# Performance work log

Hardware: AMD Instinct MI355X
Metric: run time of the kernel (lower is better)

The kernel has to match this reference:

```python
import jax, jax.numpy as jnp
import numpy as np

N, E, F_IN, H_MID, D_OUT = 20000, 320000, 1024, 256, 128
SCALE_PARAM = 3.0
LEAKY_SLOPE = 0.01


def setup_inputs() -> dict:
    key = jax.random.key(0)
    ks = jax.random.split(key, 12)
    inv = lambda k, i, o: jax.random.normal(k, (i, o), jnp.float32) / np.sqrt(i)
    return {
        "x": jax.random.normal(ks[0], (N, F_IN), jnp.float32),
        "edge_index": jax.random.randint(ks[1], (2, E), 0, N, dtype=jnp.int64),
        "W_gcn": inv(ks[2], F_IN, H_MID),
        "b_gcn": jnp.zeros((H_MID,), jnp.float32),
        "Wq": inv(ks[3], H_MID, D_OUT), "bq": jnp.zeros((D_OUT,), jnp.float32),
        "Wk": inv(ks[4], H_MID, D_OUT), "bk": jnp.zeros((D_OUT,), jnp.float32),
        "Wv": inv(ks[5], H_MID, D_OUT), "bv": jnp.zeros((D_OUT,), jnp.float32),
        "Ws": inv(ks[6], H_MID, D_OUT), "bs": jnp.zeros((D_OUT,), jnp.float32),
    }


def reference(x, edge_index, W_gcn, b_gcn, Wq, bq, Wk, bk, Wv, bv, Ws, bs):
    n = x.shape[0]
    src, dst = edge_index[0], edge_index[1]  # message flows src(j) -> dst(i)

    # ---- GCNConv(feature_dim -> inter_dim), add_self_loops=True, sym norm ----
    loop = jnp.arange(n, dtype=src.dtype)
    row = jnp.concatenate([src, loop])
    col = jnp.concatenate([dst, loop])
    deg = jax.ops.segment_sum(jnp.ones(row.shape, x.dtype), col, num_segments=n)
    dinv = jnp.where(deg > 0, jax.lax.rsqrt(deg), 0.0)
    norm = dinv[row] * dinv[col]                      # [E+N]
    h = x @ W_gcn                                     # [N, H_MID]
    h = jax.ops.segment_sum(h[row] * norm[:, None], col, num_segments=n) + b_gcn
    h = jnp.where(h >= 0, h, LEAKY_SLOPE * h)         # LeakyReLU
    # Dropout(p) is identity at inference.

    # ---- TransformerConvReducrLayer (heads=1, no self loops, sigmoid score) ----
    d = Wq.shape[1]
    q = h @ Wq + bq
    k = h @ Wk + bk
    v = h @ Wv + bv
    alpha = jnp.sum(q[dst] * k[src], axis=-1) / jnp.sqrt(jnp.asarray(d, h.dtype))  # [E]
    alpha = alpha - alpha.mean()
    alpha = alpha / ((1.0 / SCALE_PARAM) * jnp.std(alpha, ddof=1))  # torch unbiased std
    alpha = jax.nn.sigmoid(alpha)
    msg = v[src] * alpha[:, None]                     # [E, D_OUT]
    out = jax.ops.segment_sum(msg, dst, num_segments=n)
    out = out + (h @ Ws + bs)                         # root_weight skip (PyG default)
    return out
```

## Files before the change

### kernel.cpp

```cpp
#include <hip/hip_runtime.h>
#include <hip/hip_bf16.h>

#define NNODES 20000
#define EEDGES 320000
#define FIN 1024
#define HMID 256
#define DOUT 128
#define ALPHA_BLOCKS ((NNODES + 3) / 4)

typedef __bf16 bf16x8 __attribute__((ext_vector_type(8)));
typedef __bf16 bf16x4 __attribute__((ext_vector_type(4)));
typedef __bf16 bf16x2 __attribute__((ext_vector_type(2)));
typedef float f32x4 __attribute__((ext_vector_type(4)));

typedef const __attribute__((address_space(1))) void* gas_ptr;
typedef __attribute__((address_space(3))) void* las_ptr;
__device__ __forceinline__ void async_copy16(const void* g, void* l) {
    __builtin_amdgcn_global_load_lds((gas_ptr)g, (las_ptr)l, 16, 0, 0);
}

__device__ __forceinline__ float readlane_f(float v, int lane) {
    return __uint_as_float(__builtin_amdgcn_readlane(__float_as_uint(v), lane));
}

__global__ void k_pack_w(const float* __restrict__ W, __bf16* __restrict__ Wtp) {
    int tid = blockIdx.x * 256 + threadIdx.x;
    int kk = tid >> 10;
    int rem = tid & 1023;
    int h = rem >> 9;
    int u = rem & 511;
    int kq = u >> 7, c = u & 127;
    int col = h * 128 + c;
    int k0 = kk * 32 + kq * 8;
    bf16x8 v;
#pragma unroll
    for (int j = 0; j < 8; j++)
        v[j] = (__bf16)W[(size_t)(k0 + j) * HMID + col];
    *(bf16x8*)(Wtp + (size_t)tid * 8) = v;
}

__global__ void k_prep_watt(const float* __restrict__ Wq, const float* __restrict__ Wk,
                            const float* __restrict__ Wv, const float* __restrict__ Ws,
                            const float* __restrict__ bq, const float* __restrict__ bk,
                            const float* __restrict__ bv, const float* __restrict__ bs,
                            __bf16* __restrict__ Wallt, float* __restrict__ ball) {
    int g = blockIdx.y;
    const float* W = (g == 0) ? Wq : (g == 1) ? Wk : (g == 2) ? Wv : Ws;
    int tid = blockIdx.x * 256 + threadIdx.x;
    int n = tid & 127;
    int k0u = tid >> 7;
    if (k0u < 32) {
        bf16x8 v;
#pragma unroll
        for (int j = 0; j < 8; j++)
            v[j] = (__bf16)W[(size_t)(k0u * 8 + j) * DOUT + n];
        *(bf16x8*)(Wallt + (size_t)(g * DOUT + n) * HMID + k0u * 8) = v;
    }
    if (tid < DOUT) {
        const float* b = (g == 0) ? bq : (g == 1) ? bk : (g == 2) ? bv : bs;
        ball[g * DOUT + tid] = b[tid];
    }
}

__global__ void k_init(int* __restrict__ cnt, float* __restrict__ S) {
    int i = blockIdx.x * 256 + threadIdx.x;
    if (i < NNODES) cnt[i] = 0;
    if (i < 16) S[i] = 0.0f;
}

__global__ void k_count(const int* __restrict__ dst, int* __restrict__ cnt) {
    int e = blockIdx.x * 256 + threadIdx.x;
    if (e < EEDGES) atomicAdd(&cnt[dst[e]], 1);
}

__global__ void k_dinv(const int* __restrict__ cnt, float* __restrict__ dinv,
                       int* __restrict__ cursor) {
    int i = blockIdx.x * 256 + threadIdx.x;
    if (i < NNODES) {
        dinv[i] = rsqrtf((float)cnt[i] + 1.0f);
        cursor[i] = 0;
    }
}

__global__ __launch_bounds__(1024) void k_scan(const int* __restrict__ cnt,
                                               int* __restrict__ rowptr) {
    __shared__ int sh[1024];
    int t = threadIdx.x;
    int base = t * 20;
    int local[20];
    int sum = 0;
#pragma unroll
    for (int j = 0; j < 20; j++) {
        int i = base + j;
        int v = (i < NNODES) ? cnt[i] : 0;
        local[j] = sum;
        sum += v;
    }
    sh[t] = sum;
    __syncthreads();
    for (int off = 1; off < 1024; off <<= 1) {
        int v = (t >= off) ? sh[t - off] : 0;
        __syncthreads();
        sh[t] += v;
        __syncthreads();
    }
    int prev = (t > 0) ? sh[t - 1] : 0;
#pragma unroll
    for (int j = 0; j < 20; j++) {
        int i = base + j;
        if (i < NNODES) rowptr[i] = prev + local[j];
    }
    if (t == 1023) rowptr[NNODES] = sh[1023];
}

__global__ void k_fill(const int* __restrict__ src, const int* __restrict__ dst,
                       const int* __restrict__ rowptr, int* __restrict__ cursor,
                       const float* __restrict__ dinv,
                       int* __restrict__ srcsorted, float* __restrict__ wsorted) {
    int e = blockIdx.x * 256 + threadIdx.x;
    if (e >= EEDGES) return;
    int d = dst[e];
    int s = src[e];
    int pos = atomicAdd(&cursor[d], 1);
    int w = rowptr[d] + pos;
    srcsorted[w] = s;
    wsorted[w] = dinv[s];
}

__global__ __launch_bounds__(256) void k_gemm1(const float* __restrict__ x,
                                               const __bf16* __restrict__ Wtp,
                                               __bf16* __restrict__ h0bf) {
    __shared__ __bf16 As[1024];
    __shared__ __bf16 Bs[4096];
    int t = threadIdx.x;
    int lane = t & 63;
    int m = lane & 15, q = lane >> 4;
    int w = t >> 6;
    int wc = w * 32;
    int r0 = blockIdx.x * 32;
    int h = blockIdx.y;
    int c0 = h * 128;

    int arow = t >> 3;
    const float* ap = x + (size_t)(r0 + arow) * FIN + (t & 7) * 4;
    __bf16* awr = &As[arow * 32 + ((t & 7) >> 1) * 8 + (t & 1) * 4];
    const __bf16* bb = Wtp + (size_t)h * 4096;

    f32x4 acc[2][2] = {};

    float4 a = *(const float4*)(ap);

#pragma unroll 1
    for (int kk = 0; kk < 32; kk++) {
        async_copy16(bb + (size_t)kk * 8192 + t * 8, &Bs[t * 8]);
        async_copy16(bb + (size_t)kk * 8192 + (t + 256) * 8, &Bs[(t + 256) * 8]);
        bf16x4 av;
        av[0] = (__bf16)a.x; av[1] = (__bf16)a.y; av[2] = (__bf16)a.z; av[3] = (__bf16)a.w;
        *(bf16x4*)awr = av;
        if (kk + 1 < 32) a = *(const float4*)(ap + (kk + 1) * 32);
        __syncthreads();

        bf16x8 af[2], bfr[2];
#pragma unroll
        for (int i = 0; i < 2; i++)
            af[i] = *(const bf16x8*)&As[(i * 16 + m) * 32 + q * 8];
#pragma unroll
        for (int jb = 0; jb < 2; jb++)
            bfr[jb] = *(const bf16x8*)&Bs[(q * 128 + wc + jb * 16 + m) * 8];
#pragma unroll
        for (int i = 0; i < 2; i++)
#pragma unroll
            for (int jb = 0; jb < 2; jb++)
                acc[i][jb] = __builtin_amdgcn_mfma_f32_16x16x32_bf16(af[i], bfr[jb], acc[i][jb], 0, 0, 0);
        __syncthreads();
    }

#pragma unroll
    for (int i = 0; i < 2; i++)
#pragma unroll
        for (int jb = 0; jb < 2; jb++)
#pragma unroll
            for (int r = 0; r < 4; r++) {
                int row = r0 + i * 16 + q * 4 + r;
                int col = c0 + wc + jb * 16 + m;
                h0bf[(size_t)row * 256 + col] = (__bf16)acc[i][jb][r];
            }
}

__global__ __launch_bounds__(256) void k_gcn_gather(const int* __restrict__ rowptr,
                                                    const int* __restrict__ srcsorted,
                                                    const float* __restrict__ wsorted,
                                                    const __bf16* __restrict__ h0bf,
                                                    const float* __restrict__ dinv,
                                                    const float* __restrict__ bgcn,
                                                    __bf16* __restrict__ hbf) {
    int gid = blockIdx.x * 256 + threadIdx.x;
    int n = gid >> 6, l = gid & 63;
    if (n >= NNODES) return;
    float dn = dinv[n];
    float wn = dn * dn;
    bf16x4 hv = *(const bf16x4*)(h0bf + (size_t)n * 256 + l * 4);
    float4 b = ((const float4*)bgcn)[l];
    float ax = (float)hv[0] * wn + b.x;
    float ay = (float)hv[1] * wn + b.y;
    float az = (float)hv[2] * wn + b.z;
    float aw = (float)hv[3] * wn + b.w;
    int beg = rowptr[n], end = rowptr[n + 1];
    int deg = end - beg;
    int degc = deg < 64 ? deg : 64;

    int sidx = 0; float swt = 0.f;
    if (l < degc) {
        sidx = srcsorted[beg + l];
        swt = wsorted[beg + l] * dn;
    }

    for (int e0 = 0; e0 < degc; e0 += 8) {
#pragma unroll
        for (int j = 0; j < 8; j++) {
            int e = e0 + j;
            if (e >= degc) break;
            int s = __builtin_amdgcn_readlane(sidx, e);
            float wv = readlane_f(swt, e);
            bf16x4 v = *(const bf16x4*)(h0bf + (size_t)s * 256 + l * 4);
            ax += (float)v[0] * wv;
            ay += (float)v[1] * wv;
            az += (float)v[2] * wv;
            aw += (float)v[3] * wv;
        }
    }
    for (int i = beg + 64; i < end; i++) {
        int s = srcsorted[i];
        float wv = wsorted[i] * dn;
        bf16x4 v = *(const bf16x4*)(h0bf + (size_t)s * 256 + l * 4);
        ax += (float)v[0] * wv;
        ay += (float)v[1] * wv;
        az += (float)v[2] * wv;
        aw += (float)v[3] * wv;
    }
    bf16x4 o;
    o[0] = (__bf16)(ax >= 0.f ? ax : 0.01f * ax);
    o[1] = (__bf16)(ay >= 0.f ? ay : 0.01f * ay);
    o[2] = (__bf16)(az >= 0.f ? az : 0.01f * az);
    o[3] = (__bf16)(aw >= 0.f ? aw : 0.01f * aw);
    *(bf16x4*)(hbf + (size_t)n * 256 + l * 4) = o;
}

__global__ __launch_bounds__(256) void k_gemm2(const __bf16* __restrict__ hbf,
                                               const __bf16* __restrict__ Wallt,
                                               const float* __restrict__ ball,
                                               __bf16* __restrict__ qarr,
                                               __bf16* __restrict__ karr,
                                               __bf16* __restrict__ varr,
                                               __bf16* __restrict__ sarr) {
    __shared__ __bf16 As[2048];
    __shared__ __bf16 Bs[4096];
    int t = threadIdx.x;
    int lane = t & 63;
    int m = lane & 15, q = lane >> 4;
    int wave = t >> 6;
    int wr = (wave & 1) * 32;
    int wc = (wave >> 1) * 64;
    int r0 = blockIdx.x * 64;
    int c0 = blockIdx.y * 128;
    __bf16* tbl = (blockIdx.y == 0) ? qarr : (blockIdx.y == 1) ? karr
                : (blockIdx.y == 2) ? varr : sarr;

    int arow = r0 + (t & 63);
    if (arow >= NNODES) arow = NNODES - 1;
    const __bf16* asrc = hbf + (size_t)arow * HMID + (t >> 6) * 8;
    __bf16* aldst = &As[(size_t)t * 8];
    int u1 = t + 256;
    const __bf16* bsrc0 = Wallt + (size_t)(c0 + (t & 127)) * HMID + (t >> 7) * 8;
    __bf16* bldst0 = &Bs[(size_t)t * 8];
    const __bf16* bsrc1 = Wallt + (size_t)(c0 + (u1 & 127)) * HMID + (u1 >> 7) * 8;
    __bf16* bldst1 = &Bs[(size_t)u1 * 8];

    f32x4 acc[2][4] = {};

    for (int k0 = 0; k0 < HMID; k0 += 32) {
        async_copy16(asrc + k0, aldst);
        async_copy16(bsrc0 + k0, bldst0);
        async_copy16(bsrc1 + k0, bldst1);
        __syncthreads();

        bf16x8 af[2], bfr[4];
#pragma unroll
        for (int i = 0; i < 2; i++)
            af[i] = *(const bf16x8*)&As[(size_t)(q * 64 + wr + i * 16 + m) * 8];
#pragma unroll
        for (int jb = 0; jb < 4; jb++)
            bfr[jb] = *(const bf16x8*)&Bs[(size_t)(q * 128 + wc + jb * 16 + m) * 8];
#pragma unroll
        for (int i = 0; i < 2; i++)
#pragma unroll
            for (int jb = 0; jb < 4; jb++)
                acc[i][jb] = __builtin_amdgcn_mfma_f32_16x16x32_bf16(af[i], bfr[jb], acc[i][jb], 0, 0, 0);
        __syncthreads();
    }

#pragma unroll
    for (int jb = 0; jb < 4; jb++) {
        int dcol = wc + jb * 16 + m;
        float bias = ball[c0 + dcol];
#pragma unroll
        for (int i = 0; i < 2; i++)
#pragma unroll
            for (int r = 0; r < 4; r++) {
                int row = r0 + wr + i * 16 + q * 4 + r;
                if (row < NNODES) tbl[(size_t)row * 128 + dcol] = (__bf16)(acc[i][jb][r] + bias);
            }
    }
}

__global__ __launch_bounds__(256) void k_alpha(const int* __restrict__ rowptr,
                                               const int* __restrict__ srcsorted,
                                               const __bf16* __restrict__ qarr,
                                               const __bf16* __restrict__ karr,
                                               float* __restrict__ alpha,
                                               float* __restrict__ part) {
    int n = (blockIdx.x * 256 + threadIdx.x) >> 6;
    int lane = threadIdx.x & 63;
    int g = lane >> 4, l = lane & 15;
    float s1 = 0.f, s2 = 0.f;
    if (n < NNODES) {
        bf16x8 qb = *(const bf16x8*)(qarr + (size_t)n * 128 + l * 8);
        float qf[8];
#pragma unroll
        for (int j = 0; j < 8; j++) qf[j] = (float)qb[j];
        int beg = rowptr[n], end = rowptr[n + 1];
        for (int i = beg + g; i < end; i += 16) {
            int i1 = i + 4 < end ? i + 4 : end - 1;
            int i2 = i + 8 < end ? i + 8 : end - 1;
            int i3 = i + 12 < end ? i + 12 : end - 1;
            int s0 = srcsorted[i], sA = srcsorted[i1], sB = srcsorted[i2], sC = srcsorted[i3];
            bf16x8 k0 = *(const bf16x8*)(karr + (size_t)s0 * 128 + l * 8);
            bf16x8 k1 = *(const bf16x8*)(karr + (size_t)sA * 128 + l * 8);
            bf16x8 k2 = *(const bf16x8*)(karr + (size_t)sB * 128 + l * 8);
            bf16x8 k3 = *(const bf16x8*)(karr + (size_t)sC * 128 + l * 8);
            float d0 = 0.f, d1 = 0.f, d2 = 0.f, d3 = 0.f;
#pragma unroll
            for (int j = 0; j < 8; j++) {
                d0 += qf[j] * (float)k0[j];
                d1 += qf[j] * (float)k1[j];
                d2 += qf[j] * (float)k2[j];
                d3 += qf[j] * (float)k3[j];
            }
#pragma unroll
            for (int off = 1; off < 16; off <<= 1) {
                d0 += __shfl_xor(d0, off, 64);
                d1 += __shfl_xor(d1, off, 64);
                d2 += __shfl_xor(d2, off, 64);
                d3 += __shfl_xor(d3, off, 64);
            }
            if (l == 0) {
                const float sc = 0.08838834764831845f;
                float a0 = d0 * sc;
                alpha[i] = a0; s1 += a0; s2 += a0 * a0;
                if (i + 4 < end)  { float a = d1 * sc; alpha[i + 4]  = a; s1 += a; s2 += a * a; }
                if (i + 8 < end)  { float a = d2 * sc; alpha[i + 8]  = a; s1 += a; s2 += a * a; }
                if (i + 12 < end) { float a = d3 * sc; alpha[i + 12] = a; s1 += a; s2 += a * a; }
            }
        }
    }
#pragma unroll
    for (int off = 1; off < 64; off <<= 1) {
        s1 += __shfl_xor(s1, off, 64);
        s2 += __shfl_xor(s2, off, 64);
    }
    __shared__ float sh[8];
    int wave = threadIdx.x >> 6;
    if ((threadIdx.x & 63) == 0) { sh[wave] = s1; sh[4 + wave] = s2; }
    __syncthreads();
    if (threadIdx.x == 0) {
        part[2 * blockIdx.x]     = sh[0] + sh[1] + sh[2] + sh[3];
        part[2 * blockIdx.x + 1] = sh[4] + sh[5] + sh[6] + sh[7];
    }
}

__global__ __launch_bounds__(1024) void k_stats(const float* __restrict__ part,
                                                float* __restrict__ S) {
    float s1 = 0.f, s2 = 0.f;
    for (int i = threadIdx.x; i < ALPHA_BLOCKS; i += 1024) {
        s1 += part[2 * i];
        s2 += part[2 * i + 1];
    }
#pragma unroll
    for (int off = 1; off < 64; off <<= 1) {
        s1 += __shfl_xor(s1, off, 64);
        s2 += __shfl_xor(s2, off, 64);
    }
    __shared__ float sh1[16], sh2[16];
    int wave = threadIdx.x >> 6;
    if ((threadIdx.x & 63) == 0) { sh1[wave] = s1; sh2[wave] = s2; }
    __syncthreads();
    if (threadIdx.x == 0) {
        float t1 = 0.f, t2 = 0.f;
#pragma unroll
        for (int w = 0; w < 16; w++) { t1 += sh1[w]; t2 += sh2[w]; }
        float mean = t1 / (float)EEDGES;
        float var = (t2 - (float)EEDGES * mean * mean) / (float)(EEDGES - 1);
        float stdv = sqrtf(fmaxf(var, 1e-20f));
        S[2] = mean;
        S[3] = 3.0f / stdv;
    }
}

__global__ __launch_bounds__(256) void k_msg_gather(const int* __restrict__ rowptr,
                                                    const int* __restrict__ srcsorted,
                                                    const __bf16* __restrict__ varr,
                                                    const __bf16* __restrict__ sarr,
                                                    const float* __restrict__ alpha,
                                                    const float* __restrict__ S,
                                                    float* __restrict__ out) {
    int n = (blockIdx.x * 256 + threadIdx.x) >> 6;
    int l = threadIdx.x & 63;
    if (n >= NNODES) return;
    float mean = S[2], scl = S[3];
    bf16x2 sb = *(const bf16x2*)(sarr + (size_t)n * 128 + l * 2);
    float ax = (float)sb[0], ay = (float)sb[1];
    int beg = rowptr[n], end = rowptr[n + 1];
    int deg = end - beg;
    int degc = deg < 64 ? deg : 64;

    int sidx = 0; float gate = 0.f;
    if (l < degc) {
        sidx = srcsorted[beg + l];
        float z = (alpha[beg + l] - mean) * scl;
        gate = 1.0f / (1.0f + __expf(-z));
    }

    for (int e0 = 0; e0 < degc; e0 += 8) {
#pragma unroll
        for (int j = 0; j < 8; j++) {
            int e = e0 + j;
            if (e >= degc) break;
            int s = __builtin_amdgcn_readlane(sidx, e);
            float gv = readlane_f(gate, e);
            bf16x2 v = *(const bf16x2*)(varr + (size_t)s * 128 + l * 2);
            ax += (float)v[0] * gv;
            ay += (float)v[1] * gv;
        }
    }
    for (int i = beg + 64; i < end; i++) {
        int s = srcsorted[i];
        float z = (alpha[i] - mean) * scl;
        float gv = 1.0f / (1.0f + __expf(-z));
        bf16x2 v = *(const bf16x2*)(varr + (size_t)s * 128 + l * 2);
        ax += (float)v[0] * gv;
        ay += (float)v[1] * gv;
    }
    float2 o; o.x = ax; o.y = ay;
    ((float2*)(out + (size_t)n * DOUT))[l] = o;
}

extern "C" void kernel_launch(void* const* d_in, const int* in_sizes, int n_in,
                              void* d_out, int out_size, void* d_ws, size_t ws_size,
                              hipStream_t stream) {
    const float* x  = (const float*)d_in[0];
    const int* ei   = (const int*)d_in[1];
    const int* srcI = ei;
    const int* dstI = ei + EEDGES;
    const float* Wg = (const float*)d_in[2];
    const float* bg = (const float*)d_in[3];
    const float* Wq = (const float*)d_in[4];  const float* bq = (const float*)d_in[5];
    const float* Wk = (const float*)d_in[6];  const float* bk = (const float*)d_in[7];
    const float* Wv = (const float*)d_in[8];  const float* bv = (const float*)d_in[9];
    const float* Ws = (const float*)d_in[10]; const float* bs = (const float*)d_in[11];
    float* out = (float*)d_out;

    char* wsb = (char*)d_ws;
    size_t off = 0;
    auto alloc = [&](size_t bytes) -> void* {
        void* p = wsb + off;
        off += (bytes + 255) & ~(size_t)255;
        return p;
    };
    int*    cnt    = (int*)alloc((size_t)NNODES * 4);
    int*    rowptr = (int*)alloc((size_t)(NNODES + 1) * 4);
    int*    cursor = (int*)alloc((size_t)NNODES * 4);
    int*    srcst  = (int*)alloc((size_t)EEDGES * 4);
    float*  wsort  = (float*)alloc((size_t)EEDGES * 4);
    float*  dinv   = (float*)alloc((size_t)NNODES * 4);
    float*  S      = (float*)alloc(64);
    float*  part   = (float*)alloc((size_t)ALPHA_BLOCKS * 2 * 4);
    __bf16* Wtp    = (__bf16*)alloc((size_t)32 * 8192 * 2);
    __bf16* Wallt  = (__bf16*)alloc((size_t)512 * HMID * 2);
    float*  ball   = (float*)alloc(512 * 4);
    __bf16* h0bf   = (__bf16*)alloc((size_t)NNODES * HMID * 2);
    __bf16* hbf    = (__bf16*)alloc((size_t)NNODES * HMID * 2);
    __bf16* qarr   = (__bf16*)alloc((size_t)NNODES * 128 * 2);
    __bf16* karr   = (__bf16*)alloc((size_t)NNODES * 128 * 2);
    __bf16* varr   = (__bf16*)alloc((size_t)NNODES * 128 * 2);
    __bf16* sarr   = (__bf16*)alloc((size_t)NNODES * 128 * 2);
    float*  alphab = (float*)alloc((size_t)EEDGES * 4);
    if (off > ws_size) return;

    k_pack_w<<<128, 256, 0, stream>>>(Wg, Wtp);
    dim3 gw(16, 4);
    k_prep_watt<<<gw, 256, 0, stream>>>(Wq, Wk, Wv, Ws, bq, bk, bv, bs, Wallt, ball);

    k_init<<<(NNODES + 255) / 256, 256, 0, stream>>>(cnt, S);
    k_count<<<(EEDGES + 255) / 256, 256, 0, stream>>>(dstI, cnt);
    k_dinv<<<(NNODES + 255) / 256, 256, 0, stream>>>(cnt, dinv, cursor);
    k_scan<<<1, 1024, 0, stream>>>(cnt, rowptr);
    k_fill<<<(EEDGES + 255) / 256, 256, 0, stream>>>(srcI, dstI, rowptr, cursor, dinv, srcst, wsort);

    dim3 g1(625, 2);
    k_gemm1<<<g1, 256, 0, stream>>>(x, Wtp, h0bf);

    k_gcn_gather<<<(NNODES * 64 + 255) / 256, 256, 0, stream>>>(rowptr, srcst, wsort, h0bf, dinv, bg, hbf);

    dim3 g2(313, 4);
    k_gemm2<<<g2, 256, 0, stream>>>(hbf, Wallt, ball, qarr, karr, varr, sarr);

    k_alpha<<<ALPHA_BLOCKS, 256, 0, stream>>>(rowptr, srcst, qarr, karr, alphab, part);
    k_stats<<<1, 1024, 0, stream>>>(part, S);

    k_msg_gather<<<(NNODES * 64 + 255) / 256, 256, 0, stream>>>(rowptr, srcst, varr, sarr, alphab, S, out);
}
```

Measured before the change: 314.5 us.

## Fuse small setup kernels and stats reduction to cut launch count

Merges weight packing, attention-weight prep and counter init into one kernel, folds dinv/cursor init into the scan, co-launches the CSR fill with the first GEMM grid, and computes the alpha statistics in the last finishing k_alpha block via an atomic counter. This removes several kernel launches and their inter-kernel gaps. The last-block pattern relies on threadfence ordering and a counter stored in the zeroed S buffer.

```diff
diff --git a/kernel.cpp b/kernel.cpp
--- a/kernel.cpp
+++ b/kernel.cpp
@@ -23,49 +23,49 @@
     return __uint_as_float(__builtin_amdgcn_readlane(__float_as_uint(v), lane));
 }
 
-__global__ void k_pack_w(const float* __restrict__ W, __bf16* __restrict__ Wtp) {
-    int tid = blockIdx.x * 256 + threadIdx.x;
-    int kk = tid >> 10;
-    int rem = tid & 1023;
-    int h = rem >> 9;
-    int u = rem & 511;
-    int kq = u >> 7, c = u & 127;
-    int col = h * 128 + c;
-    int k0 = kk * 32 + kq * 8;
-    bf16x8 v;
-#pragma unroll
-    for (int j = 0; j < 8; j++)
-        v[j] = (__bf16)W[(size_t)(k0 + j) * HMID + col];
-    *(bf16x8*)(Wtp + (size_t)tid * 8) = v;
-}
-
-__global__ void k_prep_watt(const float* __restrict__ Wq, const float* __restrict__ Wk,
-                            const float* __restrict__ Wv, const float* __restrict__ Ws,
-                            const float* __restrict__ bq, const float* __restrict__ bk,
-                            const float* __restrict__ bv, const float* __restrict__ bs,
-                            __bf16* __restrict__ Wallt, float* __restrict__ ball) {
-    int g = blockIdx.y;
-    const float* W = (g == 0) ? Wq : (g == 1) ? Wk : (g == 2) ? Wv : Ws;
-    int tid = blockIdx.x * 256 + threadIdx.x;
-    int n = tid & 127;
-    int k0u = tid >> 7;
-    if (k0u < 32) {
+__global__ __launch_bounds__(256) void k_prep(const float* __restrict__ Wg,
+                                              const float* __restrict__ Wq, const float* __restrict__ Wk,
+                                              const float* __restrict__ Wv, const float* __restrict__ Ws,
+                                              const float* __restrict__ bq, const float* __restrict__ bk,
+                                              const float* __restrict__ bv, const float* __restrict__ bs,
+                                              __bf16* __restrict__ Wtp, __bf16* __restrict__ Wallt,
+                                              float* __restrict__ ball,
+                                              int* __restrict__ cnt, float* __restrict__ S) {
+    int b = blockIdx.x;
+    if (b < 128) {
+        int tid = b * 256 + threadIdx.x;
+        int kk = tid >> 10;
+        int rem = tid & 1023;
+        int h = rem >> 9;
+        int u = rem & 511;
+        int kq = u >> 7, c = u & 127;
+        int col = h * 128 + c;
+        int k0 = kk * 32 + kq * 8;
+        bf16x8 v;
+#pragma unroll
+        for (int j = 0; j < 8; j++)
+            v[j] = (__bf16)Wg[(size_t)(k0 + j) * HMID + col];
+        *(bf16x8*)(Wtp + (size_t)tid * 8) = v;
+    } else if (b < 192) {
+        int g = (b - 128) >> 4;
+        const float* W = (g == 0) ? Wq : (g == 1) ? Wk : (g == 2) ? Wv : Ws;
+        int tid = ((b - 128) & 15) * 256 + threadIdx.x;
+        int n = tid & 127;
+        int k0u = tid >> 7;
         bf16x8 v;
 #pragma unroll
         for (int j = 0; j < 8; j++)
             v[j] = (__bf16)W[(size_t)(k0u * 8 + j) * DOUT + n];
         *(bf16x8*)(Wallt + (size_t)(g * DOUT + n) * HMID + k0u * 8) = v;
-    }
-    if (tid < DOUT) {
-        const float* b = (g == 0) ? bq : (g == 1) ? bk : (g == 2) ? bv : bs;
-        ball[g * DOUT + tid] = b[tid];
-    }
-}
-
-__global__ void k_init(int* __restrict__ cnt, float* __restrict__ S) {
-    int i = blockIdx.x * 256 + threadIdx.x;
-    if (i < NNODES) cnt[i] = 0;
-    if (i < 16) S[i] = 0.0f;
+        if (tid < DOUT) {
+            const float* bb = (g == 0) ? bq : (g == 1) ? bk : (g == 2) ? bv : bs;
+            ball[g * DOUT + tid] = bb[tid];
+        }
+    } else {
+        int i = (b - 192) * 256 + threadIdx.x;
+        if (i < NNODES) cnt[i] = 0;
+        if (i < 16) S[i] = 0.0f;
+    }
 }
 
 __global__ void k_count(const int* __restrict__ dst, int* __restrict__ cnt) {
@@ -73,17 +73,10 @@
     if (e < EEDGES) atomicAdd(&cnt[dst[e]], 1);
 }
 
-__global__ void k_dinv(const int* __restrict__ cnt, float* __restrict__ dinv,
-                       int* __restrict__ cursor) {
-    int i = blockIdx.x * 256 + threadIdx.x;
-    if (i < NNODES) {
-        dinv[i] = rsqrtf((float)cnt[i] + 1.0f);
-        cursor[i] = 0;
-    }
-}
-
 __global__ __launch_bounds__(1024) void k_scan(const int* __restrict__ cnt,
-                                               int* __restrict__ rowptr) {
+                                               int* __restrict__ rowptr,
+                                               float* __restrict__ dinv,
+                                               int* __restrict__ cursor) {
     __shared__ int sh[1024];
     int t = threadIdx.x;
     int base = t * 20;
@@ -93,6 +86,10 @@
     for (int j = 0; j < 20; j++) {
         int i = base + j;
         int v = (i < NNODES) ? cnt[i] : 0;
+        if (i < NNODES) {
+            dinv[i] = rsqrtf((float)v + 1.0f);
+            cursor[i] = 0;
+        }
         local[j] = sum;
         sum += v;
     }
@@ -113,32 +110,38 @@
     if (t == 1023) rowptr[NNODES] = sh[1023];
 }
 
-__global__ void k_fill(const int* __restrict__ src, const int* __restrict__ dst,
-                       const int* __restrict__ rowptr, int* __restrict__ cursor,
-                       const float* __restrict__ dinv,
-                       int* __restrict__ srcsorted, float* __restrict__ wsorted) {
-    int e = blockIdx.x * 256 + threadIdx.x;
-    if (e >= EEDGES) return;
-    int d = dst[e];
-    int s = src[e];
-    int pos = atomicAdd(&cursor[d], 1);
-    int w = rowptr[d] + pos;
-    srcsorted[w] = s;
-    wsorted[w] = dinv[s];
-}
-
-__global__ __launch_bounds__(256) void k_gemm1(const float* __restrict__ x,
-                                               const __bf16* __restrict__ Wtp,
-                                               __bf16* __restrict__ h0bf) {
+__global__ __launch_bounds__(256) void k_fill_gemm1(const float* __restrict__ x,
+                                                    const __bf16* __restrict__ Wtp,
+                                                    __bf16* __restrict__ h0bf,
+                                                    const int* __restrict__ src,
+                                                    const int* __restrict__ dst,
+                                                    const int* __restrict__ rowptr,
+                                                    int* __restrict__ cursor,
+                                                    const float* __restrict__ dinv,
+                                                    int* __restrict__ srcsorted,
+                                                    float* __restrict__ wsorted) {
     __shared__ __bf16 As[1024];
     __shared__ __bf16 Bs[4096];
+    int b = blockIdx.x;
+    if (b >= 1250) {
+        int e = (b - 1250) * 256 + threadIdx.x;
+        if (e < EEDGES) {
+            int d = dst[e];
+            int s = src[e];
+            int pos = atomicAdd(&cursor[d], 1);
+            int w = rowptr[d] + pos;
+            srcsorted[w] = s;
+            wsorted[w] = dinv[s];
+        }
+        return;
+    }
     int t = threadIdx.x;
     int lane = t & 63;
     int m = lane & 15, q = lane >> 4;
     int w = t >> 6;
     int wc = w * 32;
-    int r0 = blockIdx.x * 32;
-    int h = blockIdx.y;
+    int r0 = (b >> 1) * 32;
+    int h = b & 1;
     int c0 = h * 128;
 
     int arow = t >> 3;
@@ -318,7 +321,9 @@
                                                const __bf16* __restrict__ qarr,
                                                const __bf16* __restrict__ karr,
                                                float* __restrict__ alpha,
-                                               float* __restrict__ part) {
+                                               float* __restrict__ part,
+                                               int* __restrict__ ctr,
+                                               float* __restrict__ S) {
     int n = (blockIdx.x * 256 + threadIdx.x) >> 6;
     int lane = threadIdx.x & 63;
     int g = lane >> 4, l = lane & 15;
@@ -369,40 +374,42 @@
         s2 += __shfl_xor(s2, off, 64);
     }
     __shared__ float sh[8];
+    __shared__ int lastFlag;
     int wave = threadIdx.x >> 6;
     if ((threadIdx.x & 63) == 0) { sh[wave] = s1; sh[4 + wave] = s2; }
     __syncthreads();
     if (threadIdx.x == 0) {
         part[2 * blockIdx.x]     = sh[0] + sh[1] + sh[2] + sh[3];
         part[2 * blockIdx.x + 1] = sh[4] + sh[5] + sh[6] + sh[7];
-    }
-}
-
-__global__ __launch_bounds__(1024) void k_stats(const float* __restrict__ part,
-                                                float* __restrict__ S) {
-    float s1 = 0.f, s2 = 0.f;
-    for (int i = threadIdx.x; i < ALPHA_BLOCKS; i += 1024) {
-        s1 += part[2 * i];
-        s2 += part[2 * i + 1];
-    }
-#pragma unroll
-    for (int off = 1; off < 64; off <<= 1) {
-        s1 += __shfl_xor(s1, off, 64);
-        s2 += __shfl_xor(s2, off, 64);
-    }
-    __shared__ float sh1[16], sh2[16];
-    int wave = threadIdx.x >> 6;
-    if ((threadIdx.x & 63) == 0) { sh1[wave] = s1; sh2[wave] = s2; }
+        __threadfence();
+        int prev = atomicAdd(ctr, 1);
+        lastFlag = (prev == ALPHA_BLOCKS - 1) ? 1 : 0;
+    }
     __syncthreads();
-    if (threadIdx.x == 0) {
+    if (lastFlag) {
+        __threadfence();
         float t1 = 0.f, t2 = 0.f;
-#pragma unroll
-        for (int w = 0; w < 16; w++) { t1 += sh1[w]; t2 += sh2[w]; }
-        float mean = t1 / (float)EEDGES;
-        float var = (t2 - (float)EEDGES * mean * mean) / (float)(EEDGES - 1);
-        float stdv = sqrtf(fmaxf(var, 1e-20f));
-        S[2] = mean;
-        S[3] = 3.0f / stdv;
+        for (int i = threadIdx.x; i < ALPHA_BLOCKS; i += 256) {
+            t1 += part[2 * i];
+            t2 += part[2 * i + 1];
+        }
+#pragma unroll
+        for (int off = 1; off < 64; off <<= 1) {
+            t1 += __shfl_xor(t1, off, 64);
+            t2 += __shfl_xor(t2, off, 64);
+        }
+        __syncthreads();
+        if ((threadIdx.x & 63) == 0) { sh[wave] = t1; sh[4 + wave] = t2; }
+        __syncthreads();
+        if (threadIdx.x == 0) {
+            float u1 = sh[0] + sh[1] + sh[2] + sh[3];
+            float u2 = sh[4] + sh[5] + sh[6] + sh[7];
+            float mean = u1 / (float)EEDGES;
+            float var = (u2 - (float)EEDGES * mean * mean) / (float)(EEDGES - 1);
+            float stdv = sqrtf(fmaxf(var, 1e-20f));
+            S[2] = mean;
+            S[3] = 3.0f / stdv;
+        }
     }
 }
 
@@ -496,26 +503,21 @@
     float*  alphab = (float*)alloc((size_t)EEDGES * 4);
     if (off > ws_size) return;
 
-    k_pack_w<<<128, 256, 0, stream>>>(Wg, Wtp);
-    dim3 gw(16, 4);
-    k_prep_watt<<<gw, 256, 0, stream>>>(Wq, Wk, Wv, Ws, bq, bk, bv, bs, Wallt, ball);
-
-    k_init<<<(NNODES + 255) / 256, 256, 0, stream>>>(cnt, S);
-    k_count<<<(EEDGES + 255) / 256, 256, 0, stream>>>(dstI, cnt);
-    k_dinv<<<(NNODES + 255) / 256, 256, 0, stream>>>(cnt, dinv, cursor);
-    k_scan<<<1, 1024, 0, stream>>>(cnt, rowptr);
-    k_fill<<<(EEDGES + 255) / 256, 256, 0, stream>>>(srcI, dstI, rowptr, cursor, dinv, srcst, wsort);
-
-    dim3 g1(625, 2);
-    k_gemm1<<<g1, 256, 0, stream>>>(x, Wtp, h0bf);
-
-    k_gcn_gather<<<(NNODES * 64 + 255) / 256, 256, 0, stream>>>(rowptr, srcst, wsort, h0bf, dinv, bg, hbf);
+    k_prep<<<271, 256, 0, stream>>>(Wg, Wq, Wk, Wv, Ws, bq, bk, bv, bs,
+                                    Wtp, Wallt, ball, cnt, S);
+    k_count<<<1250, 256, 0, stream>>>(dstI, cnt);
+    k_scan<<<1, 1024, 0, stream>>>(cnt, rowptr, dinv, cursor);
+
+    k_fill_gemm1<<<2500, 256, 0, stream>>>(x, Wtp, h0bf, srcI, dstI, rowptr, cursor,
+                                           dinv, srcst, wsort);
+
+    k_gcn_gather<<<5000, 256, 0, stream>>>(rowptr, srcst, wsort, h0bf, dinv, bg, hbf);
 
     dim3 g2(313, 4);
     k_gemm2<<<g2, 256, 0, stream>>>(hbf, Wallt, ball, qarr, karr, varr, sarr);
 
-    k_alpha<<<ALPHA_BLOCKS, 256, 0, stream>>>(rowptr, srcst, qarr, karr, alphab, part);
-    k_stats<<<1, 1024, 0, stream>>>(part, S);
-
-    k_msg_gather<<<(NNODES * 64 + 255) / 256, 256, 0, stream>>>(rowptr, srcst, varr, sarr, alphab, S, out);
-}
+    k_alpha<<<ALPHA_BLOCKS, 256, 0, stream>>>(rowptr, srcst, qarr, karr, alphab, part,
+                                              (int*)S + 15, S);
+
+    k_msg_gather<<<5000, 256, 0, stream>>>(rowptr, srcst, varr, sarr, alphab, S, out);
+}
```

New measurement: 458.2 us. 1.46x slower.

## Merge prep kernels, fold dinv into scan, split GCN gather into column halves

Applied to the files above, without the earlier changes.

Merges the weight-packing, attention-weight prep and init kernels into one launch, and computes dinv and resets cursor inside the scan kernel, cutting three launches. The GCN gather is split into two launches, each covering half of the 256 feature columns (2 bf16 per lane). This shrinks the per-pass gather working set so more of it stays in cache. The cost is reading the CSR indices twice and narrower per-lane loads.

```diff
diff --git a/kernel.cpp b/kernel.cpp
--- a/kernel.cpp
+++ b/kernel.cpp
@@ -23,49 +23,49 @@
     return __uint_as_float(__builtin_amdgcn_readlane(__float_as_uint(v), lane));
 }
 
-__global__ void k_pack_w(const float* __restrict__ W, __bf16* __restrict__ Wtp) {
-    int tid = blockIdx.x * 256 + threadIdx.x;
-    int kk = tid >> 10;
-    int rem = tid & 1023;
-    int h = rem >> 9;
-    int u = rem & 511;
-    int kq = u >> 7, c = u & 127;
-    int col = h * 128 + c;
-    int k0 = kk * 32 + kq * 8;
-    bf16x8 v;
-#pragma unroll
-    for (int j = 0; j < 8; j++)
-        v[j] = (__bf16)W[(size_t)(k0 + j) * HMID + col];
-    *(bf16x8*)(Wtp + (size_t)tid * 8) = v;
-}
-
-__global__ void k_prep_watt(const float* __restrict__ Wq, const float* __restrict__ Wk,
-                            const float* __restrict__ Wv, const float* __restrict__ Ws,
-                            const float* __restrict__ bq, const float* __restrict__ bk,
-                            const float* __restrict__ bv, const float* __restrict__ bs,
-                            __bf16* __restrict__ Wallt, float* __restrict__ ball) {
-    int g = blockIdx.y;
-    const float* W = (g == 0) ? Wq : (g == 1) ? Wk : (g == 2) ? Wv : Ws;
-    int tid = blockIdx.x * 256 + threadIdx.x;
-    int n = tid & 127;
-    int k0u = tid >> 7;
-    if (k0u < 32) {
+__global__ __launch_bounds__(256) void k_prep(const float* __restrict__ Wg,
+                                              const float* __restrict__ Wq, const float* __restrict__ Wk,
+                                              const float* __restrict__ Wv, const float* __restrict__ Ws,
+                                              const float* __restrict__ bq, const float* __restrict__ bk,
+                                              const float* __restrict__ bv, const float* __restrict__ bs,
+                                              __bf16* __restrict__ Wtp, __bf16* __restrict__ Wallt,
+                                              float* __restrict__ ball,
+                                              int* __restrict__ cnt, float* __restrict__ S) {
+    int b = blockIdx.x;
+    if (b < 128) {
+        int tid = b * 256 + threadIdx.x;
+        int kk = tid >> 10;
+        int rem = tid & 1023;
+        int h = rem >> 9;
+        int u = rem & 511;
+        int kq = u >> 7, c = u & 127;
+        int col = h * 128 + c;
+        int k0 = kk * 32 + kq * 8;
+        bf16x8 v;
+#pragma unroll
+        for (int j = 0; j < 8; j++)
+            v[j] = (__bf16)Wg[(size_t)(k0 + j) * HMID + col];
+        *(bf16x8*)(Wtp + (size_t)tid * 8) = v;
+    } else if (b < 192) {
+        int g = (b - 128) >> 4;
+        const float* W = (g == 0) ? Wq : (g == 1) ? Wk : (g == 2) ? Wv : Ws;
+        int tid = ((b - 128) & 15) * 256 + threadIdx.x;
+        int n = tid & 127;
+        int k0u = tid >> 7;
         bf16x8 v;
 #pragma unroll
         for (int j = 0; j < 8; j++)
             v[j] = (__bf16)W[(size_t)(k0u * 8 + j) * DOUT + n];
         *(bf16x8*)(Wallt + (size_t)(g * DOUT + n) * HMID + k0u * 8) = v;
-    }
-    if (tid < DOUT) {
-        const float* b = (g == 0) ? bq : (g == 1) ? bk : (g == 2) ? bv : bs;
-        ball[g * DOUT + tid] = b[tid];
-    }
-}
-
-__global__ void k_init(int* __restrict__ cnt, float* __restrict__ S) {
-    int i = blockIdx.x * 256 + threadIdx.x;
-    if (i < NNODES) cnt[i] = 0;
-    if (i < 16) S[i] = 0.0f;
+        if (tid < DOUT) {
+            const float* bb = (g == 0) ? bq : (g == 1) ? bk : (g == 2) ? bv : bs;
+            ball[g * DOUT + tid] = bb[tid];
+        }
+    } else {
+        int i = (b - 192) * 256 + threadIdx.x;
+        if (i < NNODES) cnt[i] = 0;
+        if (i < 16) S[i] = 0.0f;
+    }
 }
 
 __global__ void k_count(const int* __restrict__ dst, int* __restrict__ cnt) {
@@ -73,17 +73,10 @@
     if (e < EEDGES) atomicAdd(&cnt[dst[e]], 1);
 }
 
-__global__ void k_dinv(const int* __restrict__ cnt, float* __restrict__ dinv,
-                       int* __restrict__ cursor) {
-    int i = blockIdx.x * 256 + threadIdx.x;
-    if (i < NNODES) {
-        dinv[i] = rsqrtf((float)cnt[i] + 1.0f);
-        cursor[i] = 0;
-    }
-}
-
 __global__ __launch_bounds__(1024) void k_scan(const int* __restrict__ cnt,
-                                               int* __restrict__ rowptr) {
+                                               int* __restrict__ rowptr,
+                                               float* __restrict__ dinv,
+                                               int* __restrict__ cursor) {
     __shared__ int sh[1024];
     int t = threadIdx.x;
     int base = t * 20;
@@ -93,6 +86,10 @@
     for (int j = 0; j < 20; j++) {
         int i = base + j;
         int v = (i < NNODES) ? cnt[i] : 0;
+        if (i < NNODES) {
+            dinv[i] = rsqrtf((float)v + 1.0f);
+            cursor[i] = 0;
+        }
         local[j] = sum;
         sum += v;
     }
@@ -193,18 +190,18 @@
                                                     const __bf16* __restrict__ h0bf,
                                                     const float* __restrict__ dinv,
                                                     const float* __restrict__ bgcn,
-                                                    __bf16* __restrict__ hbf) {
+                                                    __bf16* __restrict__ hbf,
+                                                    int ch) {
     int gid = blockIdx.x * 256 + threadIdx.x;
     int n = gid >> 6, l = gid & 63;
     if (n >= NNODES) return;
     float dn = dinv[n];
     float wn = dn * dn;
-    bf16x4 hv = *(const bf16x4*)(h0bf + (size_t)n * 256 + l * 4);
-    float4 b = ((const float4*)bgcn)[l];
+    int cb = ch * 128 + l * 2;
+    bf16x2 hv = *(const bf16x2*)(h0bf + (size_t)n * 256 + cb);
+    float2 b = ((const float2*)bgcn)[ch * 64 + l];
     float ax = (float)hv[0] * wn + b.x;
     float ay = (float)hv[1] * wn + b.y;
-    float az = (float)hv[2] * wn + b.z;
-    float aw = (float)hv[3] * wn + b.w;
     int beg = rowptr[n], end = rowptr[n + 1];
     int deg = end - beg;
     int degc = deg < 64 ? deg : 64;
@@ -222,28 +219,22 @@
             if (e >= degc) break;
             int s = __builtin_amdgcn_readlane(sidx, e);
             float wv = readlane_f(swt, e);
-            bf16x4 v = *(const bf16x4*)(h0bf + (size_t)s * 256 + l * 4);
+            bf16x2 v = *(const bf16x2*)(h0bf + (size_t)s * 256 + cb);
             ax += (float)v[0] * wv;
             ay += (float)v[1] * wv;
-            az += (float)v[2] * wv;
-            aw += (float)v[3] * wv;
         }
     }
     for (int i = beg + 64; i < end; i++) {
         int s = srcsorted[i];
         float wv = wsorted[i] * dn;
-        bf16x4 v = *(const bf16x4*)(h0bf + (size_t)s * 256 + l * 4);
+        bf16x2 v = *(const bf16x2*)(h0bf + (size_t)s * 256 + cb);
         ax += (float)v[0] * wv;
         ay += (float)v[1] * wv;
-        az += (float)v[2] * wv;
-        aw += (float)v[3] * wv;
-    }
-    bf16x4 o;
+    }
+    bf16x2 o;
     o[0] = (__bf16)(ax >= 0.f ? ax : 0.01f * ax);
     o[1] = (__bf16)(ay >= 0.f ? ay : 0.01f * ay);
-    o[2] = (__bf16)(az >= 0.f ? az : 0.01f * az);
-    o[3] = (__bf16)(aw >= 0.f ? aw : 0.01f * aw);
-    *(bf16x4*)(hbf + (size_t)n * 256 + l * 4) = o;
+    *(bf16x2*)(hbf + (size_t)n * 256 + cb) = o;
 }
 
 __global__ __launch_bounds__(256) void k_gemm2(const __bf16* __restrict__ hbf,
@@ -496,20 +487,17 @@
     float*  alphab = (float*)alloc((size_t)EEDGES * 4);
     if (off > ws_size) return;
 
-    k_pack_w<<<128, 256, 0, stream>>>(Wg, Wtp);
-    dim3 gw(16, 4);
-    k_prep_watt<<<gw, 256, 0, stream>>>(Wq, Wk, Wv, Ws, bq, bk, bv, bs, Wallt, ball);
-
-    k_init<<<(NNODES + 255) / 256, 256, 0, stream>>>(cnt, S);
-    k_count<<<(EEDGES + 255) / 256, 256, 0, stream>>>(dstI, cnt);
-    k_dinv<<<(NNODES + 255) / 256, 256, 0, stream>>>(cnt, dinv, cursor);
-    k_scan<<<1, 1024, 0, stream>>>(cnt, rowptr);
-    k_fill<<<(EEDGES + 255) / 256, 256, 0, stream>>>(srcI, dstI, rowptr, cursor, dinv, srcst, wsort);
+    k_prep<<<271, 256, 0, stream>>>(Wg, Wq, Wk, Wv, Ws, bq, bk, bv, bs,
+                                    Wtp, Wallt, ball, cnt, S);
+    k_count<<<1250, 256, 0, stream>>>(dstI, cnt);
+    k_scan<<<1, 1024, 0, stream>>>(cnt, rowptr, dinv, cursor);
+    k_fill<<<1250, 256, 0, stream>>>(srcI, dstI, rowptr, cursor, dinv, srcst, wsort);
 
     dim3 g1(625, 2);
     k_gemm1<<<g1, 256, 0, stream>>>(x, Wtp, h0bf);
 
-    k_gcn_gather<<<(NNODES * 64 + 255) / 256, 256, 0, stream>>>(rowptr, srcst, wsort, h0bf, dinv, bg, hbf);
+    k_gcn_gather<<<5000, 256, 0, stream>>>(rowptr, srcst, wsort, h0bf, dinv, bg, hbf, 0);
+    k_gcn_gather<<<5000, 256, 0, stream>>>(rowptr, srcst, wsort, h0bf, dinv, bg, hbf, 1);
 
     dim3 g2(313, 4);
     k_gemm2<<<g2, 256, 0, stream>>>(hbf, Wallt, ball, qarr, karr, varr, sarr);
@@ -517,5 +505,5 @@
     k_alpha<<<ALPHA_BLOCKS, 256, 0, stream>>>(rowptr, srcst, qarr, karr, alphab, part);
     k_stats<<<1, 1024, 0, stream>>>(part, S);
 
-    k_msg_gather<<<(NNODES * 64 + 255) / 256, 256, 0, stream>>>(rowptr, srcst, varr, sarr, alphab, S, out);
-}
+    k_msg_gather<<<5000, 256, 0, stream>>>(rowptr, srcst, varr, sarr, alphab, S, out);
+}
```

Result: slower. 350.9 us (+11.6%).
